# Kernel optimization log

Measured on AMD Instinct MI355X. Metric: run time of the kernel, lower is better.

The kernel has to match this reference:

```python
import jax, jax.numpy as jnp
import numpy as np

N = 96                       # max_num_nodes
T = N * (N + 1) // 2         # upper-triangular vector length
E = 256                      # embedding_dim
MAX_ITERS = 50


def setup_inputs() -> dict:
    key = jax.random.key(0)
    ks = jax.random.split(key, 8)
    graph_embedding = jax.random.normal(ks[0], (1, E), jnp.float32)
    a = (jax.random.uniform(ks[1], (1, N, N)) < 0.1).astype(jnp.float32)
    adj = jnp.maximum(a, jnp.swapaxes(a, 1, 2))  # symmetric 0/1 adjacency
    mask = jnp.ones((1, N), bool)
    W1 = jax.random.normal(ks[2], (E, 250), jnp.float32) * 0.08
    b1 = jnp.zeros((250,), jnp.float32)
    W2 = jax.random.normal(ks[3], (250, 100), jnp.float32) * 0.10
    b2 = jnp.zeros((100,), jnp.float32)
    W3 = jax.random.normal(ks[4], (100, T), jnp.float32) * 0.15
    b3 = jnp.zeros((T,), jnp.float32)
    return dict(graph_embedding=graph_embedding, adj=adj, mask=mask,
                W1=W1, b1=b1, W2=W2, b2=b2, W3=W3, b3=b3)


def _forward(graph_embedding, adj, mask, W1, b1, W2, b2, W3, b3):
    idx = jnp.arange(N)
    eye = jnp.eye(N, dtype=adj.dtype)

    # decoder: Linear -> Linear -> ReLU -> Linear -> sigmoid
    h = graph_embedding @ W1 + b1
    h = jax.nn.relu(h @ W2 + b2)
    l = jax.nn.sigmoid(h @ W3 + b3)[0]              # [T]

    # recover_adj_lower + recover_full_adj_from_lower
    iu = jnp.triu_indices(N)
    up = jnp.zeros((N, N), l.dtype).at[iu].set(l)    # row-major triu fill, as torch bool-mask assign
    recon = up + up.T - jnp.diag(jnp.diag(up))       # [N, N]
    fr = recon.sum(axis=1)                           # recon degree features

    # ori_adj with diagonal forced to 1 where mask
    a0 = adj[0]
    m = mask[0]
    ori = a0.at[idx, idx].set(jnp.where(m, jnp.asarray(1.0, a0.dtype), jnp.diag(a0)))
    f = ori.sum(axis=1)                              # ori degree features

    # edge_similarity_matrix, vectorized
    # off-diagonal block: S[i,j,a,b] = A[i,j]A[i,i]A[j,j] * R[a,b]R[a,a]R[b,b]  (i!=j, a!=b)
    dA = jnp.diag(ori)
    dR = jnp.diag(recon)
    t1 = (1.0 - eye) * ori * dA[:, None] * dA[None, :]      # [N, N], zero on diag
    t2 = (1.0 - eye) * recon * dR[:, None] * dR[None, :]    # [N, N], zero on diag
    S = t1[:, :, None, None] * t2[None, None, :, :]          # [N, N, N, N]
    # diagonal block: S[i,i,a,a] = A[i,i]R[a,a] / (|f_i - fr_a| + 1)
    sim = 1.0 / (jnp.abs(f[:, None] - fr[None, :]) + 1.0)    # [N, N]
    D = dA[:, None] * dR[None, :] * sim                      # [N, N]
    S = S.at[idx[:, None], idx[:, None], idx[None, :], idx[None, :]].set(D)

    # mpm: iterative max-pooling matching
    x0 = jnp.full((N, N), 1.0 / N, dtype=S.dtype)
    off_mask = (1.0 - eye)[:, :, None]                       # exclude j == i

    def step(x, _):
        pooled = jnp.max(x[None, :, None, :] * S, axis=3)    # [i, j, a] = max_b x[j,b]*S[i,j,a,b]
        neigh = (off_mask * pooled).sum(axis=1)              # [i, a]
        x_new = x * D + neigh                                # D[i,a] == S[i,i,a,a]
        x_new = x_new / jnp.linalg.norm(x_new)
        return x_new, None

    x, _ = jax.lax.scan(step, x0, None, length=MAX_ITERS)
    return x  # soft assignment matrix [N, N]


def reference(graph_embedding, adj, mask, W1, b1, W2, b2, W3, b3):
    return _forward(graph_embedding, adj, mask, W1, b1, W2, b2, W3, b3)
```

## Files before the change

kernel.cpp:

```cpp
#include <hip/hip_runtime.h>
#include <hip/hip_bf16.h>

#define NN 96
#define NB 32
#define NTH 256
#define RPB 3
#define NITER 50
#define SMASK 0x8000000080000000ULL
#define SPIN_MAX 32768
#define MAXF 32

typedef unsigned long long ull;
typedef float v2f __attribute__((ext_vector_type(2)));

__device__ __forceinline__ float bf2f(__hip_bfloat16 v){ return __bfloat162float(v); }
__device__ __forceinline__ float LD(const void* p, int i, bool f32){
  return f32 ? ((const float*)p)[i]
             : __bfloat162float(((const __hip_bfloat16*)p)[i]);
}
__device__ __forceinline__ float ldA(const float* p){
  return __hip_atomic_load(p, __ATOMIC_RELAXED, __HIP_MEMORY_SCOPE_AGENT);
}
__device__ __forceinline__ ull ldA64(const ull* p){
  return __hip_atomic_load(p, __ATOMIC_RELAXED, __HIP_MEMORY_SCOPE_AGENT);
}
__device__ __forceinline__ void stXf(float* p, float v){
  (void)__hip_atomic_exchange(p, v, __ATOMIC_RELAXED, __HIP_MEMORY_SCOPE_AGENT);
}
__device__ __forceinline__ void stX64(ull* p, ull v){
  (void)__hip_atomic_exchange(p, v, __ATOMIC_RELAXED, __HIP_MEMORY_SCOPE_AGENT);
}
__device__ __forceinline__ int ldSacq(const int* p){
  return __hip_atomic_load(p, __ATOMIC_ACQUIRE, __HIP_MEMORY_SCOPE_WORKGROUP);
}
__device__ __forceinline__ void stSrel(int* p, int v){
  __hip_atomic_store(p, v, __ATOMIC_RELEASE, __HIP_MEMORY_SCOPE_WORKGROUP);
}

__global__ __launch_bounds__(NTH, 1) void gvae(
    const void* __restrict__ ge,  const void* __restrict__ adj,
    const void* __restrict__ W1,  const void* __restrict__ b1,
    const void* __restrict__ W2,  const void* __restrict__ b2,
    const void* __restrict__ W3,  const void* __restrict__ b3,
    void* __restrict__ out, float* __restrict__ ws)
{
  __shared__ __align__(16) float t2s[NN * NN + 4600];
  __shared__ __align__(16) float stg[4656];
  __shared__ __align__(16) float xs[RPB * NN];
  __shared__ __align__(16) float Ds[RPB * NN];
  __shared__ __align__(16) float msd[4 * RPB * NN];
  __shared__ float ges[256], h1s[250], h2s[100];
  __shared__ unsigned char nbl[RPB * 96];
  __shared__ unsigned char onbl[RPB * 2];
  __shared__ int   fcnts[RPB], ocnts[RPB];
  __shared__ float fdeg[RPB];
  __shared__ float frs[NN], dRs[NN];
  __shared__ float wpart[4 * RPB];
  __shared__ int   wpstamp[4 * RPB];
  __shared__ int   rstamp[4 * RPB];
  __shared__ float sring[8];
  __shared__ int   sstamp[8];
  __shared__ int   bdone;

  const int tid = threadIdx.x, blk = blockIdx.x;

  float* pn  = ws;
  float* lg  = ws + 2048;
  ull*   Mb0 = (ull*)(ws + 8192);
  ull*   Mb1 = Mb0 + 4608;

  if (blk >= NB){
    if (tid == 0) bdone = 0;
    __syncthreads();
    const float* dn = ws + 1664;
    const int wv = tid >> 6;
    float a0 = 1.1f + blk, a1 = 2.2f, a2 = 3.3f, a3 = 4.4f;
    float a4 = 5.5f, a5 = 6.6f, a6 = 7.7f, a7 = 8.8f;
    const float m = 1.0000001f;
    for (int outer = 0; outer < 16384; ++outer){
#pragma unroll
      for (int u = 0; u < 8; ++u){
        a0 = fmaf(a0, m, 1e-6f); a1 = fmaf(a1, m, 2e-6f);
        a2 = fmaf(a2, m, 3e-6f); a3 = fmaf(a3, m, 4e-6f);
        a4 = fmaf(a4, m, 5e-6f); a5 = fmaf(a5, m, 6e-6f);
        a6 = fmaf(a6, m, 7e-6f); a7 = fmaf(a7, m, 8e-6f);
      }
      __builtin_amdgcn_s_sleep(4);
      int stop;
      if (wv == 0){
        float v = (tid == 0 && (outer & 7) == 0) ? ldA(dn) : 0.f;
        stop = __any(v > 0.5f) ? 1 : 0;
        if (stop && tid == 0)
          __hip_atomic_store(&bdone, 1, __ATOMIC_RELAXED, __HIP_MEMORY_SCOPE_WORKGROUP);
      } else {
        stop = __hip_atomic_load(&bdone, __ATOMIC_RELAXED, __HIP_MEMORY_SCOPE_WORKGROUP);
      }
      if (stop) break;
    }
    float sum = a0 + a1 + a2 + a3 + a4 + a5 + a6 + a7;
    if (sum == 0.12345678f) stXf(ws + 1700, sum);
    return;
  }

  float sv = (tid < 128) ? bf2f(((const __hip_bfloat16*)W1)[tid])
                         : bf2f(((const __hip_bfloat16*)W3)[tid - 128]);
  const bool isf32 = __syncthreads_or(!(fabsf(sv) < 1e4f)) != 0;

  if (tid < 256) ges[tid] = LD(ge, tid, isf32);
  __syncthreads();
  if (tid < 250){
    float a0 = LD(b1, tid, isf32), a1 = 0.f, a2 = 0.f, a3 = 0.f;
    for (int e = 0; e < 256; e += 4){
      a0 += ges[e]     * LD(W1, (e    ) * 250 + tid, isf32);
      a1 += ges[e + 1] * LD(W1, (e + 1) * 250 + tid, isf32);
      a2 += ges[e + 2] * LD(W1, (e + 2) * 250 + tid, isf32);
      a3 += ges[e + 3] * LD(W1, (e + 3) * 250 + tid, isf32);
    }
    h1s[tid] = (a0 + a1) + (a2 + a3);
  }
  __syncthreads();
  if (tid < 100){
    float a0 = LD(b2, tid, isf32), a1 = 0.f;
    for (int k = 0; k < 250; k += 2){
      a0 += h1s[k]     * LD(W2, (k    ) * 100 + tid, isf32);
      a1 += h1s[k + 1] * LD(W2, (k + 1) * 100 + tid, isf32);
    }
    h2s[tid] = fmaxf(a0 + a1, 0.f);
  }
  __syncthreads();

  if (tid < 146){
    int o = blk * 146 + tid;
    if (o < 4656){
      float a = LD(b3, o, isf32);
      for (int k = 0; k < 100; ++k) a += h2s[k] * LD(W3, k * 4656 + o, isf32);
      stXf(&lg[o], 1.f / (1.f + expf(-a)));
    }
  }
  if (tid >= 192 && tid < 192 + RPB){
    int r = tid - 192, ig = blk * RPB + r;
    int lo = blk * RPB, hi = lo + RPB;
    float fs = 1.f; int c = 0, co = 0;
    for (int j = 0; j < NN; ++j){
      if (j == ig) continue;
      float v = LD(adj, ig * NN + j, isf32);
      fs += v;
      if (v > 0.5f){
        if (j >= lo && j < hi) onbl[r * 2 + (co++)] = (unsigned char)(j - lo);
        else                   nbl[r * 96 + (c++)]  = (unsigned char)j;
      }
    }
    fcnts[r] = c; ocnts[r] = co; fdeg[r] = fs;
  }
  {
    float vv[19];
    unsigned pend = 0;
#pragma unroll
    for (int c = 0; c < 19; ++c) if (tid + NTH * c < 4656) pend |= 1u << c;
    int spin = 0;
    while (pend && spin++ < SPIN_MAX){
      unsigned p2 = pend;
#pragma unroll
      for (int c = 0; c < 19; ++c)
        if ((p2 >> c) & 1) vv[c] = ldA(&lg[tid + NTH * c]);
#pragma unroll
      for (int c = 0; c < 19; ++c)
        if (((p2 >> c) & 1) && vv[c] > 0.f){
          stg[tid + NTH * c] = vv[c];
          pend &= ~(1u << c);
        }
      if (pend == p2) __builtin_amdgcn_s_sleep(2);
    }
  }
  __syncthreads();

  for (int e = tid; e < NN * NN; e += NTH){
    int a = e / NN, b = e % NN, i = min(a, b), j = max(a, b);
    int k = i * NN - (i * (i - 1)) / 2 + (j - i);
    t2s[e] = stg[k];
  }
  __syncthreads();
  if (tid < NN){
    float srow = 0.f;
    for (int b = 0; b < NN; ++b) srow += t2s[b * NN + tid];
    frs[tid] = srow; dRs[tid] = t2s[tid * NN + tid];
  }
  __syncthreads();
  for (int e = tid; e < NN * NN; e += NTH){
    int a = e / NN, b = e % NN;
    t2s[e] = (a == b) ? 0.f : t2s[e] * dRs[a] * dRs[b];
  }
  for (int o = tid; o < RPB * NN; o += NTH){
    int r = o / NN, a = o % NN;
    Ds[o] = dRs[a] / (fabsf(fdeg[r] - frs[a]) + 1.f);
    xs[o] = 1.f / 96.f;
  }
  if (tid < 4 * RPB){ rstamp[tid] = -1; wpstamp[tid] = -1; }
  if (tid < 8) sstamp[tid] = -1;
  __syncthreads();

  const int wv = tid >> 6, l = tid & 63;

  if (wv < RPB){
    const int g = blk * RPB + wv;
    const bool act = (l < 48);
    const int p = l;
    int fc = 0, nf = 0, gw = 0;
    int off[MAXF];
    const int oc  = ocnts[wv];
    const int ow0 = onbl[wv * 2], ow1 = onbl[wv * 2 + 1];
    if (act){
      fc = fcnts[wv]; nf = fc < MAXF ? fc : MAXF;
      gw = g * 48 + p;
#pragma unroll
      for (int c = 0; c < MAXF; ++c)
        off[c] = (c < nf) ? ((int)nbl[wv * 96 + c] * 48 + p) : gw;
    }

    for (int it = 0; it < NITER; ++it){
      ull* Mw = (it & 1) ? Mb1 : Mb0;
      const ull sg = ((it >> 1) & 1) ? SMASK : 0ULL;
      const int ring = (it & 3) * RPB;

      float mx = 0.f, my = 0.f;
      if (act){
        v2f m0 = {0.f, 0.f}, m1 = {0.f, 0.f};
        v2f m2 = {0.f, 0.f}, m3 = {0.f, 0.f};
        for (int b = 0; b < NN; b += 4){
          v2f t0 = *(const v2f*)&t2s[(b    ) * NN + 2 * p];
          v2f t1 = *(const v2f*)&t2s[(b + 1) * NN + 2 * p];
          v2f t2 = *(const v2f*)&t2s[(b + 2) * NN + 2 * p];
          v2f t3 = *(const v2f*)&t2s[(b + 3) * NN + 2 * p];
          v2f xv = *(const v2f*)&xs[wv * NN + b];
          v2f xw = *(const v2f*)&xs[wv * NN + b + 2];
          m0.x = fmaxf(m0.x, xv.x * t0.x); m0.y = fmaxf(m0.y, xv.x * t0.y);
          m1.x = fmaxf(m1.x, xv.y * t1.x); m1.y = fmaxf(m1.y, xv.y * t1.y);
          m2.x = fmaxf(m2.x, xw.x * t2.x); m2.y = fmaxf(m2.y, xw.x * t2.y);
          m3.x = fmaxf(m3.x, xw.y * t3.x); m3.y = fmaxf(m3.y, xw.y * t3.y);
        }
        mx = fmaxf(fmaxf(m0.x, m1.x), fmaxf(m2.x, m3.x));
        my = fmaxf(fmaxf(m0.y, m1.y), fmaxf(m2.y, m3.y));
        *(v2f*)&msd[(ring + wv) * NN + 2 * p] = (v2f){mx, my};
      }
      if (l == 0) stSrel(&rstamp[ring + wv], it);
      if (act){
        ull enc = (((ull)__float_as_uint(my + 1.f)) << 32) | __float_as_uint(mx + 1.f);
        stX64(&Mw[gw], enc ^ sg);
      }

      float s = 1.f;
      if (it >= 2){
        int sl = it & 7, sp = 0;
        while (ldSacq(&sstamp[sl]) != it && ++sp < SPIN_MAX)
          if ((sp & 63) == 0) __builtin_amdgcn_s_sleep(1);
        s = sring[sl];
      }

      v2f acc = {0.f, 0.f};
      if (act){
        ull vv[MAXF];
        unsigned pend = (nf >= 32) ? 0xffffffffu : ((1u << nf) - 1u);
        int spin = 0;
        while (pend && spin++ < SPIN_MAX){
          unsigned p2 = pend;
#pragma unroll
          for (int c = 0; c < MAXF; ++c)
            if ((p2 >> c) & 1) vv[c] = ldA64(&Mw[off[c]]);
#pragma unroll
          for (int c = 0; c < MAXF; ++c)
            if (((p2 >> c) & 1) && !((vv[c] ^ sg) & SMASK)) pend &= ~(1u << c);
        }
#pragma unroll
        for (int c = 0; c < MAXF; ++c)
          if (c < nf){
            acc.x += fabsf(__uint_as_float((unsigned)vv[c])) - 1.f;
            acc.y += fabsf(__uint_as_float((unsigned)(vv[c] >> 32))) - 1.f;
          }
        for (int c = MAXF; c < fc; ++c){
          int o3 = (int)nbl[wv * 96 + c] * 48 + p;
          ull w; int sp = 0;
          do { w = ldA64(&Mw[o3]); } while (((w ^ sg) & SMASK) && ++sp < SPIN_MAX);
          acc.x += fabsf(__uint_as_float((unsigned)w)) - 1.f;
          acc.y += fabsf(__uint_as_float((unsigned)(w >> 32))) - 1.f;
        }
      }
      for (int t = 0; t < oc; ++t){
        int wj = (t == 0) ? ow0 : ow1;
        int rs = ring + wj, sp = 0;
        while (ldSacq(&rstamp[rs]) != it && ++sp < SPIN_MAX){}
        if (act){
          v2f mv = *(const v2f*)&msd[rs * NN + 2 * p];
          acc.x += mv.x; acc.y += mv.y;
        }
      }

      float nsq = 0.f;
      if (act){
        v2f w2 = *(const v2f*)&xs[wv * NN + 2 * p];
        v2f d2 = *(const v2f*)&Ds[wv * NN + 2 * p];
        v2f u; u.x = s * (w2.x * d2.x + acc.x); u.y = s * (w2.y * d2.y + acc.y);
        *(v2f*)&xs[wv * NN + 2 * p] = u;
        nsq = u.x * u.x + u.y * u.y;
      }
      for (int o2 = 32; o2; o2 >>= 1) nsq += __shfl_down(nsq, o2, 64);
      if (l == 0){
        wpart[ring + wv] = nsq;
        stSrel(&wpstamp[ring + wv], it);
      }
    }
  } else {
    for (int it = 0; it <= NITER; ++it){
      if (l == 0 && it >= 1){
        int sl = ((it - 1) & 3) * RPB; float t = 0.f;
        for (int w = 0; w < RPB; ++w){
          int sp = 0;
          while (ldSacq(&wpstamp[sl + w]) != it - 1 && ++sp < SPIN_MAX)
            if ((sp & 63) == 0) __builtin_amdgcn_s_sleep(1);
          t += wpart[sl + w];
        }
        stXf(&pn[it * NB + blk], t);
      }
      if (it >= 2){
        int slot = (it == NITER) ? NITER : (it - 1);
        float v = 0.f;
        if (l < NB){
          int sp = 0;
          for (;;){
            v = ldA(&pn[slot * NB + l]);
            if (v > 0.f || ++sp >= SPIN_MAX) break;
            __builtin_amdgcn_s_sleep(1);
          }
        }
        for (int o2 = 16; o2; o2 >>= 1) v += __shfl_down(v, o2, 64);
        if (l == 0){
          sring[it & 7] = rsqrtf(v);
          stSrel(&sstamp[it & 7], it);
        }
      }
    }
  }
  __syncthreads();

  float sf = sring[NITER & 7];
  for (int o = tid; o < RPB * NN; o += NTH){
    int og = blk * RPB * NN + o;
    float v = sf * xs[o];
    if (isf32) ((float*)out)[og] = v;
    else       ((__hip_bfloat16*)out)[og] = __float2bfloat16(v);
  }
  if (blk == 0 && tid == 0) stXf(ws + 1664, 1.f);
}

extern "C" void kernel_launch(void* const* d_in, const int* in_sizes, int n_in,
                              void* d_out, int out_size, void* d_ws, size_t ws_size,
                              hipStream_t stream) {
  (void)in_sizes; (void)n_in; (void)out_size; (void)ws_size;
  hipLaunchKernelGGL(gvae, dim3(256), dim3(NTH), 0, stream,
                     d_in[0], d_in[1], d_in[3], d_in[4], d_in[5], d_in[6],
                     d_in[7], d_in[8], d_out, (float*)d_ws);
}
```

Before: 407.3 us.

## Replace global per-iteration norm with local power-of-two scaling and final normalization

Drops the grid-wide L2-norm reduction that every iteration had to wait on. Each row-wave now rescales its own vector by a power of two computed from its local norm and tracks the exponent. Neighbours publish their exponent beside their messages and receivers realign contributions with exact pow2 factors. A single global normalization runs only at the end. The message buffers grow to a 4-deep ring, so the scheme depends on exponent bookkeeping and cross-block ordering staying consistent.

```diff
diff --git a/kernel.cpp b/kernel.cpp
--- a/kernel.cpp
+++ b/kernel.cpp
@@ -9,6 +9,7 @@
 #define SMASK 0x8000000080000000ULL
 #define SPIN_MAX 32768
 #define MAXF 32
+#define MWORDS 4704
 
 typedef unsigned long long ull;
 typedef float v2f __attribute__((ext_vector_type(2)));
@@ -35,6 +36,9 @@
 }
 __device__ __forceinline__ void stSrel(int* p, int v){
   __hip_atomic_store(p, v, __ATOMIC_RELEASE, __HIP_MEMORY_SCOPE_WORKGROUP);
+}
+__device__ __forceinline__ float pow2i(int e){
+  return __int_as_float((unsigned)(127 + e) << 23);
 }
 
 __global__ __launch_bounds__(NTH, 1) void gvae(
@@ -44,30 +48,30 @@
     const void* __restrict__ W3,  const void* __restrict__ b3,
     void* __restrict__ out, float* __restrict__ ws)
 {
-  __shared__ __align__(16) float t2s[NN * NN + 4600];
+  __shared__ __align__(16) float t2s[NN * NN + 3000];
   __shared__ __align__(16) float stg[4656];
   __shared__ __align__(16) float xs[RPB * NN];
   __shared__ __align__(16) float Ds[RPB * NN];
-  __shared__ __align__(16) float msd[4 * RPB * NN];
+  __shared__ __align__(16) float msd[8 * RPB * NN];
   __shared__ float ges[256], h1s[250], h2s[100];
   __shared__ unsigned char nbl[RPB * 96];
   __shared__ unsigned char onbl[RPB * 2];
   __shared__ int   fcnts[RPB], ocnts[RPB];
   __shared__ float fdeg[RPB];
   __shared__ float frs[NN], dRs[NN];
-  __shared__ float wpart[4 * RPB];
-  __shared__ int   wpstamp[4 * RPB];
-  __shared__ int   rstamp[4 * RPB];
-  __shared__ float sring[8];
-  __shared__ int   sstamp[8];
+  __shared__ int   lss[8 * RPB];
+  __shared__ int   rstamp[8 * RPB];
+  __shared__ int   fm_sh;
+  __shared__ float fS_sh;
+  __shared__ int   fstamp;
   __shared__ int   bdone;
 
   const int tid = threadIdx.x, blk = blockIdx.x;
 
-  float* pn  = ws;
-  float* lg  = ws + 2048;
-  ull*   Mb0 = (ull*)(ws + 8192);
-  ull*   Mb1 = Mb0 + 4608;
+  float* lg   = ws + 2048;
+  float* finA = ws + 6720;
+  float* finB = ws + 6848;
+  ull*   Mbase = (ull*)(ws + 8192);
 
   if (blk >= NB){
     if (tid == 0) bdone = 0;
@@ -106,7 +110,7 @@
                          : bf2f(((const __hip_bfloat16*)W3)[tid - 128]);
   const bool isf32 = __syncthreads_or(!(fabsf(sv) < 1e4f)) != 0;
 
-  if (tid < 256) ges[tid] = LD(ge, tid, isf32);
+  ges[tid] = LD(ge, tid, isf32);
   __syncthreads();
   if (tid < 250){
     float a0 = LD(b1, tid, isf32), a1 = 0.f, a2 = 0.f, a3 = 0.f;
@@ -195,8 +199,8 @@
     Ds[o] = dRs[a] / (fabsf(fdeg[r] - frs[a]) + 1.f);
     xs[o] = 1.f / 96.f;
   }
-  if (tid < 4 * RPB){ rstamp[tid] = -1; wpstamp[tid] = -1; }
-  if (tid < 8) sstamp[tid] = -1;
+  if (tid < 8 * RPB){ rstamp[tid] = -1; lss[tid] = 0; }
+  if (tid == 0) fstamp = -1;
   __syncthreads();
 
   const int wv = tid >> 6, l = tid & 63;
@@ -207,6 +211,7 @@
     const int p = l;
     int fc = 0, nf = 0, gw = 0;
     int off[MAXF];
+    int scaddr = 0;
     const int oc  = ocnts[wv];
     const int ow0 = onbl[wv * 2], ow1 = onbl[wv * 2 + 1];
     if (act){
@@ -215,12 +220,15 @@
 #pragma unroll
       for (int c = 0; c < MAXF; ++c)
         off[c] = (c < nf) ? ((int)nbl[wv * 96 + c] * 48 + p) : gw;
-    }
+      scaddr = 4608 + ((l < nf) ? (int)nbl[wv * 96 + l] : g);
+    }
+    int ls = 0;
+    float fn2 = 1.f;
 
     for (int it = 0; it < NITER; ++it){
-      ull* Mw = (it & 1) ? Mb1 : Mb0;
-      const ull sg = ((it >> 1) & 1) ? SMASK : 0ULL;
-      const int ring = (it & 3) * RPB;
+      ull* Mw = Mbase + (it & 3) * MWORDS;
+      const ull sg = ((it >> 2) & 1) ? SMASK : 0ULL;
+      const int ring = (it & 7) * RPB;
 
       float mx = 0.f, my = 0.f;
       if (act){
@@ -242,113 +250,136 @@
         my = fmaxf(fmaxf(m0.y, m1.y), fmaxf(m2.y, m3.y));
         *(v2f*)&msd[(ring + wv) * NN + 2 * p] = (v2f){mx, my};
       }
-      if (l == 0) stSrel(&rstamp[ring + wv], it);
+      if (l == 0){ lss[ring + wv] = ls; stSrel(&rstamp[ring + wv], it); }
       if (act){
         ull enc = (((ull)__float_as_uint(my + 1.f)) << 32) | __float_as_uint(mx + 1.f);
         stX64(&Mw[gw], enc ^ sg);
       }
-
-      float s = 1.f;
-      if (it >= 2){
-        int sl = it & 7, sp = 0;
-        while (ldSacq(&sstamp[sl]) != it && ++sp < SPIN_MAX)
-          if ((sp & 63) == 0) __builtin_amdgcn_s_sleep(1);
-        s = sring[sl];
+      if (l == 0){
+        unsigned es = __float_as_uint((float)ls + 16384.f);
+        stX64(&Mw[4608 + g], ((((ull)es) << 32) | es) ^ sg);
       }
 
       v2f acc = {0.f, 0.f};
-      if (act){
-        ull vv[MAXF];
+      int lsnb = 0;
+      if (act){
+        ull vv[MAXF]; ull scw = 0;
         unsigned pend = (nf >= 32) ? 0xffffffffu : ((1u << nf) - 1u);
+        int psc = (l < nf) ? 1 : 0;
         int spin = 0;
-        while (pend && spin++ < SPIN_MAX){
-          unsigned p2 = pend;
+        while ((pend || psc) && spin++ < SPIN_MAX){
+          unsigned p2 = pend; int q2 = psc;
+          if (q2) scw = ldA64(&Mw[scaddr]);
 #pragma unroll
           for (int c = 0; c < MAXF; ++c)
             if ((p2 >> c) & 1) vv[c] = ldA64(&Mw[off[c]]);
+          if (q2 && !((scw ^ sg) & SMASK)) psc = 0;
 #pragma unroll
           for (int c = 0; c < MAXF; ++c)
             if (((p2 >> c) & 1) && !((vv[c] ^ sg) & SMASK)) pend &= ~(1u << c);
         }
+        lsnb = (int)(fabsf(__uint_as_float((unsigned)scw)) - 16384.f);
 #pragma unroll
         for (int c = 0; c < MAXF; ++c)
           if (c < nf){
-            acc.x += fabsf(__uint_as_float((unsigned)vv[c])) - 1.f;
-            acc.y += fabsf(__uint_as_float((unsigned)(vv[c] >> 32))) - 1.f;
+            int dd = ls - __shfl(lsnb, c, 64);
+            float rt = pow2i(dd);
+            acc.x += rt * (fabsf(__uint_as_float((unsigned)vv[c])) - 1.f);
+            acc.y += rt * (fabsf(__uint_as_float((unsigned)(vv[c] >> 32))) - 1.f);
           }
         for (int c = MAXF; c < fc; ++c){
-          int o3 = (int)nbl[wv * 96 + c] * 48 + p;
+          int j = (int)nbl[wv * 96 + c];
           ull w; int sp = 0;
-          do { w = ldA64(&Mw[o3]); } while (((w ^ sg) & SMASK) && ++sp < SPIN_MAX);
-          acc.x += fabsf(__uint_as_float((unsigned)w)) - 1.f;
-          acc.y += fabsf(__uint_as_float((unsigned)(w >> 32))) - 1.f;
+          do { w = ldA64(&Mw[j * 48 + p]); } while (((w ^ sg) & SMASK) && ++sp < SPIN_MAX);
+          ull sw; sp = 0;
+          do { sw = ldA64(&Mw[4608 + j]); } while (((sw ^ sg) & SMASK) && ++sp < SPIN_MAX);
+          int dd = ls - (int)(fabsf(__uint_as_float((unsigned)sw)) - 16384.f);
+          float rt = pow2i(dd);
+          acc.x += rt * (fabsf(__uint_as_float((unsigned)w)) - 1.f);
+          acc.y += rt * (fabsf(__uint_as_float((unsigned)(w >> 32))) - 1.f);
         }
       }
       for (int t = 0; t < oc; ++t){
         int wj = (t == 0) ? ow0 : ow1;
         int rs = ring + wj, sp = 0;
         while (ldSacq(&rstamp[rs]) != it && ++sp < SPIN_MAX){}
+        int lj = lss[rs];
         if (act){
+          float rt = pow2i(ls - lj);
           v2f mv = *(const v2f*)&msd[rs * NN + 2 * p];
-          acc.x += mv.x; acc.y += mv.y;
-        }
-      }
-
-      float nsq = 0.f;
+          acc.x += rt * mv.x; acc.y += rt * mv.y;
+        }
+      }
+
+      float nsq = 0.f; v2f u = {0.f, 0.f};
       if (act){
         v2f w2 = *(const v2f*)&xs[wv * NN + 2 * p];
         v2f d2 = *(const v2f*)&Ds[wv * NN + 2 * p];
-        v2f u; u.x = s * (w2.x * d2.x + acc.x); u.y = s * (w2.y * d2.y + acc.y);
+        u.x = w2.x * d2.x + acc.x; u.y = w2.y * d2.y + acc.y;
+        nsq = u.x * u.x + u.y * u.y;
+      }
+      for (int o2 = 32; o2; o2 >>= 1) nsq += __shfl_xor(nsq, o2, 64);
+      nsq = __shfl(nsq, 0, 64);
+      int k = (int)roundf(0.5f * log2f(nsq));
+      float s = pow2i(-k);
+      if (act){
+        u.x *= s; u.y *= s;
         *(v2f*)&xs[wv * NN + 2 * p] = u;
-        nsq = u.x * u.x + u.y * u.y;
-      }
-      for (int o2 = 32; o2; o2 >>= 1) nsq += __shfl_down(nsq, o2, 64);
-      if (l == 0){
-        wpart[ring + wv] = nsq;
-        stSrel(&wpstamp[ring + wv], it);
-      }
-    }
+      }
+      ls -= k;
+      fn2 = nsq * s * s;
+    }
+
+    if (l == 0){
+      stXf(&finA[g], (float)ls + 16384.f);
+      stXf(&finB[g], fn2);
+    }
+    { int sp = 0;
+      while (ldSacq(&fstamp) != 1 && ++sp < SPIN_MAX)
+        if ((sp & 63) == 0) __builtin_amdgcn_s_sleep(1);
+    }
+    int dd = (-ls) - fm_sh; if (dd < -126) dd = -126;
+    float fac = pow2i(dd) * rsqrtf(fS_sh);
+    if (act){
+      v2f w2 = *(const v2f*)&xs[wv * NN + 2 * p];
+      int og = g * NN + 2 * p;
+      if (isf32){
+        ((float*)out)[og] = w2.x * fac; ((float*)out)[og + 1] = w2.y * fac;
+      } else {
+        ((__hip_bfloat16*)out)[og]     = __float2bfloat16(w2.x * fac);
+        ((__hip_bfloat16*)out)[og + 1] = __float2bfloat16(w2.y * fac);
+      }
+    }
+    if (blk == 0 && wv == 0 && l == 0) stXf(ws + 1664, 1.f);
   } else {
-    for (int it = 0; it <= NITER; ++it){
-      if (l == 0 && it >= 1){
-        int sl = ((it - 1) & 3) * RPB; float t = 0.f;
-        for (int w = 0; w < RPB; ++w){
-          int sp = 0;
-          while (ldSacq(&wpstamp[sl + w]) != it - 1 && ++sp < SPIN_MAX)
-            if ((sp & 63) == 0) __builtin_amdgcn_s_sleep(1);
-          t += wpart[sl + w];
-        }
-        stXf(&pn[it * NB + blk], t);
-      }
-      if (it >= 2){
-        int slot = (it == NITER) ? NITER : (it - 1);
-        float v = 0.f;
-        if (l < NB){
-          int sp = 0;
-          for (;;){
-            v = ldA(&pn[slot * NB + l]);
-            if (v > 0.f || ++sp >= SPIN_MAX) break;
-            __builtin_amdgcn_s_sleep(1);
-          }
-        }
-        for (int o2 = 16; o2; o2 >>= 1) v += __shfl_down(v, o2, 64);
-        if (l == 0){
-          sring[it & 7] = rsqrtf(v);
-          stSrel(&sstamp[it & 7], it);
-        }
-      }
-    }
-  }
-  __syncthreads();
-
-  float sf = sring[NITER & 7];
-  for (int o = tid; o < RPB * NN; o += NTH){
-    int og = blk * RPB * NN + o;
-    float v = sf * xs[o];
-    if (isf32) ((float*)out)[og] = v;
-    else       ((__hip_bfloat16*)out)[og] = __float2bfloat16(v);
-  }
-  if (blk == 0 && tid == 0) stXf(ws + 1664, 1.f);
+    const bool has2 = (l < 32);
+    float a1 = -1.f, a2 = -1.f, b1v = -1.f, b2v = -1.f;
+    int p1 = 1, p2m = has2 ? 1 : 0, p3 = 1, p4 = has2 ? 1 : 0;
+    int sp = 0;
+    while ((p1 | p2m | p3 | p4) && sp++ < 4 * SPIN_MAX){
+      if (p1 ){ a1  = ldA(&finA[l]);      if (a1  > 0.f) p1  = 0; }
+      if (p3 ){ b1v = ldA(&finB[l]);      if (b1v > 0.f) p3  = 0; }
+      if (p2m){ a2  = ldA(&finA[64 + l]); if (a2  > 0.f) p2m = 0; }
+      if (p4 ){ b2v = ldA(&finB[64 + l]); if (b2v > 0.f) p4  = 0; }
+      if (p1 | p2m | p3 | p4) __builtin_amdgcn_s_sleep(2);
+    }
+    int ls1 = (int)(a1 - 16384.f);
+    int ls2 = has2 ? (int)(a2 - 16384.f) : 0x7fffffff;
+    int mn = ls1 < ls2 ? ls1 : ls2;
+    for (int o2 = 32; o2; o2 >>= 1){
+      int ot = __shfl_xor(mn, o2, 64);
+      if (ot < mn) mn = ot;
+    }
+    mn = __shfl(mn, 0, 64);
+    int mneg = -mn;
+    float S = 0.f;
+    { int d1 = 2 * ((-ls1) - mneg); if (d1 < -126) d1 = -126;
+      S += b1v * pow2i(d1);
+      if (has2){ int d2i = 2 * ((-ls2) - mneg); if (d2i < -126) d2i = -126;
+        S += b2v * pow2i(d2i); } }
+    for (int o2 = 32; o2; o2 >>= 1) S += __shfl_xor(S, o2, 64);
+    if (l == 0){ fm_sh = mneg; fS_sh = S; stSrel(&fstamp, 1); }
+  }
 }
 
 extern "C" void kernel_launch(void* const* d_in, const int* in_sizes, int n_in,
```

New measurement: 519.9 us. +27.6%, slower.
